# Kernel optimization log

Hardware: AMD Instinct MI355X
Metric: run time of the kernel (lower is better)

Reference implementation:

```python
import jax, jax.numpy as jnp
import numpy as np

B, S, V, E, H, O = 128, 256, 50000, 512, 1024, 10

def setup_inputs() -> dict:
    key = jax.random.key(0)
    ks = jax.random.split(key, 16)
    sc_e = 1.0 / np.sqrt(E)
    sc_h = 1.0 / np.sqrt(H)
    inp = {
        "x": jax.random.randint(ks[0], (B, S), 0, V, dtype=jnp.int64),
        "emb": jax.random.normal(ks[1], (V, E), dtype=jnp.float32),
        "W_ii": jax.random.uniform(ks[2], (H, E), jnp.float32, -sc_e, sc_e),
        "b_ii": jax.random.uniform(ks[3], (H,), jnp.float32, -sc_e, sc_e),
        "W_hi": jax.random.uniform(ks[4], (H, H), jnp.float32, -sc_h, sc_h),
        "W_if": jax.random.uniform(ks[5], (H, E), jnp.float32, -sc_e, sc_e),
        "b_if": jax.random.uniform(ks[6], (H,), jnp.float32, -sc_e, sc_e),
        "W_hf": jax.random.uniform(ks[7], (H, H), jnp.float32, -sc_h, sc_h),
        "W_ig": jax.random.uniform(ks[8], (H, E), jnp.float32, -sc_e, sc_e),
        "b_ig": jax.random.uniform(ks[9], (H,), jnp.float32, -sc_e, sc_e),
        "W_hg": jax.random.uniform(ks[10], (H, H), jnp.float32, -sc_h, sc_h),
        "W_io": jax.random.uniform(ks[11], (H, E), jnp.float32, -sc_e, sc_e),
        "b_io": jax.random.uniform(ks[12], (H,), jnp.float32, -sc_e, sc_e),
        "W_ho": jax.random.uniform(ks[13], (H, H), jnp.float32, -sc_h, sc_h),
        "fc_W": jax.random.uniform(ks[14], (O, H), jnp.float32, -sc_h, sc_h),
        "fc_b": jax.random.uniform(ks[15], (O,), jnp.float32, -sc_h, sc_h),
    }
    return inp


def _lstm_last_h(x, emb, W_ii, b_ii, W_hi, W_if, b_if, W_hf,
                 W_ig, b_ig, W_hg, W_io, b_io, W_ho):
    e = emb[x]  # [B, S, E]
    # Precompute all input-to-gate projections in one batched GEMM each: [B, S, H]
    xi = jnp.einsum('bse,he->bsh', e, W_ii) + b_ii
    xf = jnp.einsum('bse,he->bsh', e, W_if) + b_if
    xg = jnp.einsum('bse,he->bsh', e, W_ig) + b_ig
    xo = jnp.einsum('bse,he->bsh', e, W_io) + b_io
    # time-major for scan: [S, B, H]
    gates_x = jnp.stack([xi, xf, xg, xo], axis=0).transpose(2, 0, 1, 3)  # [S, 4, B, H]

    h0 = jnp.zeros((x.shape[0], W_hi.shape[0]), dtype=e.dtype)
    c0 = jnp.zeros_like(h0)

    def step(carry, gx):
        h, c = carry
        gi, gf, gg, go = gx[0], gx[1], gx[2], gx[3]
        i_t = jax.nn.sigmoid(gi + h @ W_hi.T)
        f_t = jax.nn.sigmoid(gf + h @ W_hf.T)
        g_t = jnp.tanh(gg + h @ W_hg.T)
        o_t = jax.nn.sigmoid(go + h @ W_ho.T)
        c = f_t * c + i_t * g_t
        h = o_t * jnp.tanh(c)
        return (h, c), None

    (h_T, _), _ = jax.lax.scan(step, (h0, c0), gates_x)
    return h_T  # last hidden state [B, H]


def reference(x, emb, W_ii, b_ii, W_hi, W_if, b_if, W_hf,
              W_ig, b_ig, W_hg, W_io, b_io, W_ho, fc_W, fc_b):
    h_T = _lstm_last_h(x, emb, W_ii, b_ii, W_hi, W_if, b_if, W_hf,
                       W_ig, b_ig, W_hg, W_io, b_io, W_ho)
    return h_T @ fc_W.T + fc_b  # [B, O]
```

## Files before the change

### kernel.cpp

```cpp
#include <hip/hip_runtime.h>
#include <hip/hip_cooperative_groups.h>


typedef __attribute__((ext_vector_type(8))) _Float16 half8;
typedef __attribute__((ext_vector_type(4))) float f32x4;

#define MFMA16(a, b, c) __builtin_amdgcn_mfma_f32_16x16x32_f16((a), (b), (c), 0, 0, 0)

__device__ __forceinline__ float sigm(float x) { return 1.0f / (1.0f + __expf(-x)); }
__device__ __forceinline__ float tanh_(float x) { return 1.0f - 2.0f / (__expf(2.0f * x) + 1.0f); }


__global__ __launch_bounds__(256) void k_cast_e(const int* __restrict__ x,
                                                const float* __restrict__ emb,
                                                _Float16* __restrict__ e) {
  int idx = (blockIdx.x * 256 + threadIdx.x) * 8;
  int m = idx >> 9, k = idx & 511;
  int tok = x[m];
  const float* src = emb + (long)tok * 512 + k;
  float4 a = *(const float4*)src;
  float4 b = *(const float4*)(src + 4);
  half8 h;
  h[0] = (_Float16)a.x; h[1] = (_Float16)a.y; h[2] = (_Float16)a.z; h[3] = (_Float16)a.w;
  h[4] = (_Float16)b.x; h[5] = (_Float16)b.y; h[6] = (_Float16)b.z; h[7] = (_Float16)b.w;
  *(half8*)(e + idx) = h;
}

__global__ __launch_bounds__(256) void k_cast_wi(const float* __restrict__ Wii, const float* __restrict__ Wif,
                                                 const float* __restrict__ Wig, const float* __restrict__ Wio,
                                                 _Float16* __restrict__ Wi) {
  int idx = (blockIdx.x * 256 + threadIdx.x) * 8;
  int g = idx >> 19;
  const float* src = (g == 0) ? Wii : (g == 1) ? Wif : (g == 2) ? Wig : Wio;
  src += idx & 524287;
  float4 a = *(const float4*)src;
  float4 b = *(const float4*)(src + 4);
  half8 h;
  h[0] = (_Float16)a.x; h[1] = (_Float16)a.y; h[2] = (_Float16)a.z; h[3] = (_Float16)a.w;
  h[4] = (_Float16)b.x; h[5] = (_Float16)b.y; h[6] = (_Float16)b.z; h[7] = (_Float16)b.w;
  *(half8*)(Wi + idx) = h;
}

__global__ __launch_bounds__(256) void k_cast_wh(const float* __restrict__ Whi, const float* __restrict__ Whf,
                                                 const float* __restrict__ Whg, const float* __restrict__ Who,
                                                 _Float16* __restrict__ Wh) {
  int idx = (blockIdx.x * 256 + threadIdx.x) * 8;
  int n = idx >> 10, k = idx & 1023;
  int cg = n >> 6, rem = n & 63, g = rem >> 4, cc = rem & 15;
  const float* src = (g == 0) ? Whi : (g == 1) ? Whf : (g == 2) ? Whg : Who;
  src += (cg * 16 + cc) * 1024 + k;
  float4 a = *(const float4*)src;
  float4 b = *(const float4*)(src + 4);
  half8 h;
  h[0] = (_Float16)a.x; h[1] = (_Float16)a.y; h[2] = (_Float16)a.z; h[3] = (_Float16)a.w;
  h[4] = (_Float16)b.x; h[5] = (_Float16)b.y; h[6] = (_Float16)b.z; h[7] = (_Float16)b.w;
  *(half8*)(Wh + idx) = h;
}

__global__ __launch_bounds__(256) void k_cast_bias(const float* __restrict__ bii, const float* __restrict__ bif,
                                                   const float* __restrict__ big, const float* __restrict__ bio,
                                                   float* __restrict__ bc) {
  int n = blockIdx.x * 256 + threadIdx.x;
  int g = n >> 10, hh = n & 1023;
  const float* src = (g == 0) ? bii : (g == 1) ? bif : (g == 2) ? big : bio;
  bc[n] = src[hh];
}

__global__ void k_zero(unsigned int* p) { p[blockIdx.x * 256 + threadIdx.x] = 0u; }

__global__ __launch_bounds__(256) void k_gemm1(const _Float16* __restrict__ E, const _Float16* __restrict__ Wi,
                                               const float* __restrict__ bias, _Float16* __restrict__ gx) {
  __shared__ _Float16 As[128][40];
  __shared__ _Float16 Bs[128][40];
  const int t = threadIdx.x;
  const int bm = blockIdx.x >> 5, bn = blockIdx.x & 31;
  const int m0 = bm << 7, n0 = bn << 7;
  const int lane = t & 63, wv = t >> 6;
  const int wm = (wv >> 1) << 6, wn = (wv & 1) << 6;
  const int ln = lane & 15, q = lane >> 4;
  const int rowA0 = t >> 2, kc0 = t & 3;
  const int rowA1 = (t + 256) >> 2, kc1 = (t + 256) & 3;

  f32x4 acc[4][4] = {};

  for (int k0 = 0; k0 < 512; k0 += 32) {
    *(half8*)&As[rowA0][kc0 * 8] = *(const half8*)(E + (m0 + rowA0) * 512 + k0 + kc0 * 8);
    *(half8*)&As[rowA1][kc1 * 8] = *(const half8*)(E + (m0 + rowA1) * 512 + k0 + kc1 * 8);
    *(half8*)&Bs[rowA0][kc0 * 8] = *(const half8*)(Wi + (n0 + rowA0) * 512 + k0 + kc0 * 8);
    *(half8*)&Bs[rowA1][kc1 * 8] = *(const half8*)(Wi + (n0 + rowA1) * 512 + k0 + kc1 * 8);
    __syncthreads();
    half8 af[4], bf[4];
#pragma unroll
    for (int i = 0; i < 4; i++) af[i] = *(const half8*)&As[wm + i * 16 + ln][q * 8];
#pragma unroll
    for (int i = 0; i < 4; i++) bf[i] = *(const half8*)&Bs[wn + i * 16 + ln][q * 8];
#pragma unroll
    for (int mi = 0; mi < 4; mi++)
#pragma unroll
      for (int ni = 0; ni < 4; ni++) acc[mi][ni] = MFMA16(af[mi], bf[ni], acc[mi][ni]);
    __syncthreads();
  }

#pragma unroll
  for (int ni = 0; ni < 4; ni++) {
    int n = n0 + wn + ni * 16 + ln;
    float bv = bias[n];
    int g = n >> 10, hh = n & 1023;
#pragma unroll
    for (int mi = 0; mi < 4; mi++) {
#pragma unroll
      for (int r = 0; r < 4; r++) {
        int m = m0 + wm + mi * 16 + q * 4 + r;
        int b = m >> 8, s = m & 255;
        float v = acc[mi][ni][r] + bv;
        gx[(long)(((s << 2) | g) * 128 + b) * 1024 + hh] = (_Float16)v;
      }
    }
  }
}

__global__ __launch_bounds__(256, 1) void k_lstm(const _Float16* __restrict__ gx, const _Float16* __restrict__ Wh,
                                                 _Float16* __restrict__ hrot, float* __restrict__ hT,
                                                 unsigned int* __restrict__ bar) {
  __shared__ float pre4[2][4][4][32][17];
  const int bid = blockIdx.x;
  const int cg = bid & 63, rs = bid >> 6;
  const int r0 = rs << 5, c0 = cg << 4;
  const int t = threadIdx.x, lane = t & 63, w = t >> 6;
  const int ln = lane & 15, q = lane >> 4;
  unsigned int* grp = bar + rs * 1024;
  unsigned int* myslot = grp + ((cg << 2) + w) * 4;
  unsigned int* pslot = grp + ((((w << 4) + (lane >> 2)) << 2) + (lane & 3)) * 4;

  half8 breg[4][8];
  const _Float16* wbase = Wh + (cg * 64 + ln) * 1024 + w * 256 + q * 8;
#pragma unroll
  for (int g = 0; g < 4; g++)
#pragma unroll
    for (int ks = 0; ks < 8; ks++)
      breg[g][ks] = *(const half8*)(wbase + g * 16 * 1024 + ks * 32);

  const int e0 = t << 1;
  const int erow = e0 >> 4, ecol = e0 & 15;
  __hip_atomic_store((unsigned int*)(hrot + (r0 + erow) * 1024 + c0 + ecol), 0u,
                     __ATOMIC_RELAXED, __HIP_MEMORY_SCOPE_AGENT);
  asm volatile("s_waitcnt vmcnt(0)" ::: "memory");
  if (lane == 0)
    __hip_atomic_store(myslot, 1u, __ATOMIC_RELAXED, __HIP_MEMORY_SCOPE_AGENT);
  asm volatile("" ::: "memory");

  float nx[2][4];
  {
    const _Float16* gp = gx + (long)((0 * 4 + w) * 128 + r0) * 1024 + c0 + ln;
#pragma unroll
    for (int mi = 0; mi < 2; mi++)
#pragma unroll
      for (int r = 0; r < 4; r++) nx[mi][r] = (float)gp[(mi * 16 + q * 4 + r) * 1024];
  }

  float cst0 = 0.f, cst1 = 0.f;

  for (int s = 0; s < 256; s++) {
    {
      const unsigned int target = (unsigned int)(s + 1);
      for (;;) {
        unsigned int v = __hip_atomic_load(pslot, __ATOMIC_RELAXED, __HIP_MEMORY_SCOPE_AGENT);
        if (__all(v >= target)) break;
        __builtin_amdgcn_s_sleep(1);
      }
    }
    __builtin_amdgcn_sched_barrier(0);
    asm volatile("" ::: "memory");
    if ((s & 15) == 0) __builtin_amdgcn_fence(__ATOMIC_ACQUIRE, "agent");

    const _Float16* hcur = hrot + (s & 15) * 131072;
    _Float16* hnxt = hrot + ((s + 1) & 15) * 131072;

    half8 ha0[8], ha1[8];
    const _Float16* arow0 = hcur + (r0 + ln) * 1024 + w * 256 + q * 8;
    const _Float16* arow1 = arow0 + 16 * 1024;
#pragma unroll
    for (int ks = 0; ks < 8; ks++) {
      ha0[ks] = *(const half8*)(arow0 + ks * 32);
      ha1[ks] = *(const half8*)(arow1 + ks * 32);
    }

    f32x4 acc[4][2];
#pragma unroll
    for (int g = 0; g < 4; g++)
#pragma unroll
      for (int mi = 0; mi < 2; mi++)
#pragma unroll
        for (int r = 0; r < 4; r++) acc[g][mi][r] = (g == w) ? nx[mi][r] : 0.f;

    {
      int sp = (s < 255) ? s + 1 : 255;
      const _Float16* gp = gx + (long)((sp * 4 + w) * 128 + r0) * 1024 + c0 + ln;
#pragma unroll
      for (int mi = 0; mi < 2; mi++)
#pragma unroll
        for (int r = 0; r < 4; r++) nx[mi][r] = (float)gp[(mi * 16 + q * 4 + r) * 1024];
    }

#pragma unroll
    for (int ks = 0; ks < 8; ks++) {
#pragma unroll
      for (int g = 0; g < 4; g++) {
        acc[g][0] = MFMA16(ha0[ks], breg[g][ks], acc[g][0]);
        acc[g][1] = MFMA16(ha1[ks], breg[g][ks], acc[g][1]);
      }
    }

    const int sb = s & 1;
#pragma unroll
    for (int g = 0; g < 4; g++)
#pragma unroll
      for (int mi = 0; mi < 2; mi++)
#pragma unroll
        for (int r = 0; r < 4; r++)
          pre4[sb][w][g][mi * 16 + q * 4 + r][ln] = acc[g][mi][r];
    __syncthreads();

    float sg[4][2];
#pragma unroll
    for (int g = 0; g < 4; g++) {
      float a = 0.f, b = 0.f;
#pragma unroll
      for (int ww = 0; ww < 4; ww++) {
        a += pre4[sb][ww][g][erow][ecol];
        b += pre4[sb][ww][g][erow][ecol + 1];
      }
      sg[g][0] = a; sg[g][1] = b;
    }
    float i0 = sigm(sg[0][0]), f0 = sigm(sg[1][0]), g0 = tanh_(sg[2][0]), o0 = sigm(sg[3][0]);
    float i1 = sigm(sg[0][1]), f1 = sigm(sg[1][1]), g1 = tanh_(sg[2][1]), o1 = sigm(sg[3][1]);
    cst0 = f0 * cst0 + i0 * g0;
    cst1 = f1 * cst1 + i1 * g1;
    float h0 = o0 * tanh_(cst0);
    float h1 = o1 * tanh_(cst1);
    union { _Float16 h[2]; unsigned int u; } pk;
    pk.h[0] = (_Float16)h0; pk.h[1] = (_Float16)h1;

    if (s == 255) {
      float* hp = hT + (r0 + erow) * 1024 + c0 + ecol;
      hp[0] = h0; hp[1] = h1;
    } else {
      __hip_atomic_store((unsigned int*)(hnxt + (r0 + erow) * 1024 + c0 + ecol), pk.u,
                         __ATOMIC_RELAXED, __HIP_MEMORY_SCOPE_AGENT);
      asm volatile("s_waitcnt vmcnt(0)" ::: "memory");
      if (lane == 0)
        __hip_atomic_store(myslot, (unsigned int)(s + 2), __ATOMIC_RELAXED,
                           __HIP_MEMORY_SCOPE_AGENT);
      asm volatile("" ::: "memory");
    }
  }
}

__global__ __launch_bounds__(256) void k_fc(const float* __restrict__ hT, const float* __restrict__ W,
                                            const float* __restrict__ bias, float* __restrict__ out) {
  int gid = blockIdx.x * 4 + (threadIdx.x >> 6);
  int lane = threadIdx.x & 63;
  int b = gid / 10, o = gid - b * 10;
  const float* hp = hT + b * 1024;
  const float* wp = W + o * 1024;
  float sum = 0.f;
  for (int k = lane; k < 1024; k += 64) sum += hp[k] * wp[k];
#pragma unroll
  for (int off = 32; off > 0; off >>= 1) sum += __shfl_down(sum, off, 64);
  if (lane == 0) out[b * 10 + o] = sum + bias[o];
}

extern "C" void kernel_launch(void* const* d_in, const int* in_sizes, int n_in,
                              void* d_out, int out_size, void* d_ws, size_t ws_size,
                              hipStream_t stream) {
  const int* x = (const int*)d_in[0];
  const float* emb = (const float*)d_in[1];
  const float* Wii = (const float*)d_in[2];
  const float* bii = (const float*)d_in[3];
  const float* Whi = (const float*)d_in[4];
  const float* Wif = (const float*)d_in[5];
  const float* bif = (const float*)d_in[6];
  const float* Whf = (const float*)d_in[7];
  const float* Wig = (const float*)d_in[8];
  const float* big = (const float*)d_in[9];
  const float* Whg = (const float*)d_in[10];
  const float* Wio = (const float*)d_in[11];
  const float* bio = (const float*)d_in[12];
  const float* Who = (const float*)d_in[13];
  const float* fcW = (const float*)d_in[14];
  const float* fcb = (const float*)d_in[15];

  char* ws = (char*)d_ws;
  _Float16* gx = (_Float16*)ws;
  _Float16* E = (_Float16*)(ws + 268435456);
  _Float16* hrot = (_Float16*)(ws + 268435456);
  _Float16* WiB = (_Float16*)(ws + 301989888);
  _Float16* WhB = (_Float16*)(ws + 306184192);
  float* biasC = (float*)(ws + 314572800);
  float* hT = (float*)(ws + 315113472);
  unsigned int* bar = (unsigned int*)(ws + 315637760);
  float* out = (float*)d_out;

  k_cast_e<<<8192, 256, 0, stream>>>(x, emb, E);
  k_cast_wi<<<1024, 256, 0, stream>>>(Wii, Wif, Wig, Wio, WiB);
  k_cast_wh<<<2048, 256, 0, stream>>>(Whi, Whf, Whg, Who, WhB);
  k_cast_bias<<<16, 256, 0, stream>>>(bii, bif, big, bio, biasC);
  k_gemm1<<<8192, 256, 0, stream>>>(E, WiB, biasC, gx);
  k_zero<<<16, 256, 0, stream>>>(bar);

  const _Float16* gx_a = gx;
  const _Float16* wh_a = WhB;
  _Float16* hb_a = hrot;
  float* ht_a = hT;
  unsigned int* bar_a = bar;
  void* kargs[] = {(void*)&gx_a, (void*)&wh_a, (void*)&hb_a, (void*)&ht_a, (void*)&bar_a};
  hipLaunchCooperativeKernel(k_lstm, dim3(256), dim3(256), kargs, 0, stream);

  k_fc<<<320, 256, 0, stream>>>(hT, fcW, fcb, out);
}
```

Measured before the change: 1.907 ms.

## Use one flag per block and a block barrier for LSTM step sync

Each block now publishes a single progress flag, written by thread 0 after a __syncthreads, instead of one flag per wave written after a per-wave s_waitcnt. Pollers therefore read 64 slots (one per producer block) rather than 256 per-wave slots. Because the added barrier already orders iterations, the LDS pre-activation buffer is no longer double-buffered. The prefetch of the next step's input gates moves to after the flag publish, so it overlaps the wait, and the values are held as fp16 to save registers. The trade-off is an extra block-wide barrier in the critical path of every timestep.

```diff
diff --git a/kernel.cpp b/kernel.cpp
--- a/kernel.cpp
+++ b/kernel.cpp
@@ -122,15 +122,15 @@
 __global__ __launch_bounds__(256, 1) void k_lstm(const _Float16* __restrict__ gx, const _Float16* __restrict__ Wh,
                                                  _Float16* __restrict__ hrot, float* __restrict__ hT,
                                                  unsigned int* __restrict__ bar) {
-  __shared__ float pre4[2][4][4][32][17];
+  __shared__ float pre4[4][4][32][17];
   const int bid = blockIdx.x;
   const int cg = bid & 63, rs = bid >> 6;
   const int r0 = rs << 5, c0 = cg << 4;
   const int t = threadIdx.x, lane = t & 63, w = t >> 6;
   const int ln = lane & 15, q = lane >> 4;
   unsigned int* grp = bar + rs * 1024;
-  unsigned int* myslot = grp + ((cg << 2) + w) * 4;
-  unsigned int* pslot = grp + ((((w << 4) + (lane >> 2)) << 2) + (lane & 3)) * 4;
+  unsigned int* myslot = grp + cg * 16;
+  unsigned int* pslot = grp + ((w << 4) + (lane & 15)) * 16;
 
   half8 breg[4][8];
   const _Float16* wbase = Wh + (cg * 64 + ln) * 1024 + w * 256 + q * 8;
@@ -144,18 +144,17 @@
   const int erow = e0 >> 4, ecol = e0 & 15;
   __hip_atomic_store((unsigned int*)(hrot + (r0 + erow) * 1024 + c0 + ecol), 0u,
                      __ATOMIC_RELAXED, __HIP_MEMORY_SCOPE_AGENT);
-  asm volatile("s_waitcnt vmcnt(0)" ::: "memory");
-  if (lane == 0)
+  __syncthreads();
+  if (t == 0)
     __hip_atomic_store(myslot, 1u, __ATOMIC_RELAXED, __HIP_MEMORY_SCOPE_AGENT);
-  asm volatile("" ::: "memory");
-
-  float nx[2][4];
+
+  _Float16 nxh[2][4];
   {
     const _Float16* gp = gx + (long)((0 * 4 + w) * 128 + r0) * 1024 + c0 + ln;
 #pragma unroll
     for (int mi = 0; mi < 2; mi++)
 #pragma unroll
-      for (int r = 0; r < 4; r++) nx[mi][r] = (float)gp[(mi * 16 + q * 4 + r) * 1024];
+      for (int r = 0; r < 4; r++) nxh[mi][r] = gp[(mi * 16 + q * 4 + r) * 1024];
   }
 
   float cst0 = 0.f, cst1 = 0.f;
@@ -191,16 +190,7 @@
 #pragma unroll
       for (int mi = 0; mi < 2; mi++)
 #pragma unroll
-        for (int r = 0; r < 4; r++) acc[g][mi][r] = (g == w) ? nx[mi][r] : 0.f;
-
-    {
-      int sp = (s < 255) ? s + 1 : 255;
-      const _Float16* gp = gx + (long)((sp * 4 + w) * 128 + r0) * 1024 + c0 + ln;
-#pragma unroll
-      for (int mi = 0; mi < 2; mi++)
-#pragma unroll
-        for (int r = 0; r < 4; r++) nx[mi][r] = (float)gp[(mi * 16 + q * 4 + r) * 1024];
-    }
+        for (int r = 0; r < 4; r++) acc[g][mi][r] = (g == w) ? (float)nxh[mi][r] : 0.f;
 
 #pragma unroll
     for (int ks = 0; ks < 8; ks++) {
@@ -211,14 +201,13 @@
       }
     }
 
-    const int sb = s & 1;
 #pragma unroll
     for (int g = 0; g < 4; g++)
 #pragma unroll
       for (int mi = 0; mi < 2; mi++)
 #pragma unroll
         for (int r = 0; r < 4; r++)
-          pre4[sb][w][g][mi * 16 + q * 4 + r][ln] = acc[g][mi][r];
+          pre4[w][g][mi * 16 + q * 4 + r][ln] = acc[g][mi][r];
     __syncthreads();
 
     float sg[4][2];
@@ -227,8 +216,8 @@
       float a = 0.f, b = 0.f;
 #pragma unroll
       for (int ww = 0; ww < 4; ww++) {
-        a += pre4[sb][ww][g][erow][ecol];
-        b += pre4[sb][ww][g][erow][ecol + 1];
+        a += pre4[ww][g][erow][ecol];
+        b += pre4[ww][g][erow][ecol + 1];
       }
       sg[g][0] = a; sg[g][1] = b;
     }
@@ -247,11 +236,18 @@
     } else {
       __hip_atomic_store((unsigned int*)(hnxt + (r0 + erow) * 1024 + c0 + ecol), pk.u,
                          __ATOMIC_RELAXED, __HIP_MEMORY_SCOPE_AGENT);
-      asm volatile("s_waitcnt vmcnt(0)" ::: "memory");
-      if (lane == 0)
+      __syncthreads();
+      if (t == 0)
         __hip_atomic_store(myslot, (unsigned int)(s + 2), __ATOMIC_RELAXED,
                            __HIP_MEMORY_SCOPE_AGENT);
       asm volatile("" ::: "memory");
+      {
+        const _Float16* gp = gx + (long)(((s + 1) * 4 + w) * 128 + r0) * 1024 + c0 + ln;
+#pragma unroll
+        for (int mi = 0; mi < 2; mi++)
+#pragma unroll
+          for (int r = 0; r < 4; r++) nxh[mi][r] = gp[(mi * 16 + q * 4 + r) * 1024];
+      }
     }
   }
 }
```

Result: faster. 1.558 ms (-18.3%).
